# Kernel tuning notes

Hardware: AMD Instinct MI355X
Metric: run time of the kernel (lower is better)

Reference implementation:

```python
import jax, jax.numpy as jnp
import numpy as np

B, N, E, L = 64, 50000, 1600000, 20
BN_EPS = 1e-5


def setup_inputs() -> dict:
    key = jax.random.key(0)
    ks = jax.random.split(key, 8)
    x = jax.random.normal(ks[0], (B, N), dtype=jnp.float32)
    edge_index = jax.random.randint(ks[1], (2, E), 0, N, dtype=jnp.int32)
    alpha = jax.random.normal(ks[2], (E,), dtype=jnp.float32)
    bias = jax.random.normal(ks[3], (E,), dtype=jnp.float32)
    # LazyLinear(num_labels) on [B, N] features
    W = jax.random.normal(ks[4], (L, N), dtype=jnp.float32) / np.sqrt(N)
    b_lin = jax.random.normal(ks[5], (L,), dtype=jnp.float32) * 0.01
    # LazyBatchNorm1d affine params over N features
    gamma = jnp.ones((N,), dtype=jnp.float32)
    beta = jnp.zeros((N,), dtype=jnp.float32)
    return {"x": x, "edge_index": edge_index, "alpha": alpha, "bias": bias,
            "W": W, "b_lin": b_lin, "gamma": gamma, "beta": beta}


def reference(x, edge_index, alpha, bias, W, b_lin, gamma, beta):
    src, dst = edge_index[0], edge_index[1]
    # gather per-edge source features and apply per-edge affine: [B, E]
    x_e = alpha * x[:, src] + bias
    # scatter-mean into destination nodes: [B, N]
    sums = jnp.zeros((x.shape[0], N), dtype=x.dtype).at[:, dst].add(x_e)
    counts = jnp.zeros((N,), dtype=x.dtype).at[dst].add(1.0)
    x_hat = sums / jnp.maximum(counts, 1.0)
    out = jnp.tanh(x_hat)
    # linear head: [B, L]
    pred = x_hat @ W.T + b_lin
    # BatchNorm1d (training mode: batch stats, biased variance)
    mu = jnp.mean(out, axis=0)
    var = jnp.var(out, axis=0)
    bn = (out - mu) / jnp.sqrt(var + BN_EPS) * gamma + beta
    return (pred, bn)
```

## Files before the change

kernel.cpp:

```cpp
#include <hip/hip_runtime.h>
#include <math.h>

#define NB 64
#define NL 20
#define BN_EPS 1e-5f

#define BIN_W 32
#define NBIN 1563
#define NBINP 2048
#define BIN_CAP 1280
#define CHUNK 4096

__device__ __forceinline__ unsigned short f2bf(float f) {
    unsigned u = __float_as_uint(f);
    unsigned r = u + 0x7fff + ((u >> 16) & 1);
    return (unsigned short)(r >> 16);
}
__device__ __forceinline__ float bf2f(unsigned short h) {
    return __uint_as_float(((unsigned)h) << 16);
}

__global__ __launch_bounds__(256) void transpose_kernel(
    const float* __restrict__ x, unsigned short* __restrict__ xTb, int Nn) {
    __shared__ float tile[64][65];
    int n0 = blockIdx.x * 64;
    int ln = threadIdx.x & 63;
    int wv = threadIdx.x >> 6;
    for (int r = wv; r < 64; r += 4) {
        int col = n0 + ln;
        tile[r][ln] = (col < Nn) ? x[r * Nn + col] : 0.f;
    }
    __syncthreads();
    for (int r = wv; r < 64; r += 4) {
        int node = n0 + r;
        if (node < Nn) xTb[(size_t)node * 64 + ln] = f2bf(tile[ln][r]);
    }
}

__global__ __launch_bounds__(1024) void binsort_kernel(
    const int* __restrict__ src, const int* __restrict__ dst,
    const float* __restrict__ alpha, const float* __restrict__ bias,
    int* __restrict__ cursor, uint2* __restrict__ paybins, int E) {
    __shared__ unsigned hist[NBINP];
    __shared__ unsigned gbase[NBINP];

    int tid = threadIdx.x;
    int e0 = blockIdx.x * CHUNK;

    hist[tid] = 0;
    hist[tid + 1024] = 0;
    __syncthreads();

    uint2 pay[4];
    unsigned rk[4];
    int bn[4];
    #pragma unroll
    for (int k = 0; k < 4; ++k) {
        int e = e0 + k * 1024 + tid;
        bn[k] = -1;
        if (e < E) {
            int d = dst[e];
            int b = d >> 5;
            int dl = d & 31;
            pay[k].x = (unsigned)src[e] | ((unsigned)f2bf(alpha[e]) << 16);
            pay[k].y = (unsigned)f2bf(bias[e]) | ((unsigned)dl << 16) |
                       ((unsigned)b << 21);
            bn[k] = b;
            rk[k] = atomicAdd(&hist[b], 1u);
        }
    }
    __syncthreads();

    for (int i = tid; i < NBINP; i += 1024) {
        unsigned v = hist[i];
        if (v > 0) gbase[i] = (unsigned)atomicAdd(&cursor[i], (int)v);
    }
    __syncthreads();

    #pragma unroll
    for (int k = 0; k < 4; ++k) {
        if (bn[k] >= 0) {
            unsigned di = gbase[bn[k]] + rk[k];
            if (di < BIN_CAP)
                paybins[(size_t)bn[k] * BIN_CAP + di] = pay[k];
        }
    }
}

__global__ __launch_bounds__(256) void pull_fin3_kernel(
    const int* __restrict__ cursor, const uint2* __restrict__ paybins,
    const unsigned short* __restrict__ xTb, const float* __restrict__ W,
    const float* __restrict__ gamma, const float* __restrict__ beta,
    float* __restrict__ pred_part, float* __restrict__ bn, int Nn) {
    __shared__ __align__(16) char smem[16640];
    uint2* ed = (uint2*)smem;
    float (*xh)[65] = (float (*)[65])smem;
    float (*th)[65] = (float (*)[65])(smem + 8320);

    __shared__ float wl[NL][32];
    __shared__ unsigned h2[32], b2[32], c2[32];
    __shared__ float mu_s[32], a_s[32], be_s[32];

    int bin = blockIdx.x;
    int tid = threadIdx.x;
    int ln = tid & 63;
    int w = tid >> 6;
    int n0 = bin * 32;

    int cnt = cursor[bin];
    if (cnt > BIN_CAP) cnt = BIN_CAP;
    const uint2* pb = paybins + (size_t)bin * BIN_CAP;

    for (int i = tid; i < NL * 32; i += 256) {
        int l = i >> 5, j = i & 31;
        wl[l][j] = (n0 + j < Nn) ? W[l * Nn + n0 + j] : 0.f;
    }
    if (tid < 32) { h2[tid] = 0; c2[tid] = 0; }
    __syncthreads();

    uint2 pA = {0, 0}, pB = {0, 0}, pC = {0, 0}, pD = {0, 0}, pE = {0, 0};
    {
        int i;
        i = tid;
        if (i < cnt) { pA = pb[i]; atomicAdd(&h2[(pA.y >> 16) & 31], 1u); }
        i = tid + 256;
        if (i < cnt) { pB = pb[i]; atomicAdd(&h2[(pB.y >> 16) & 31], 1u); }
        i = tid + 512;
        if (i < cnt) { pC = pb[i]; atomicAdd(&h2[(pC.y >> 16) & 31], 1u); }
        i = tid + 768;
        if (i < cnt) { pD = pb[i]; atomicAdd(&h2[(pD.y >> 16) & 31], 1u); }
        i = tid + 1024;
        if (i < cnt) { pE = pb[i]; atomicAdd(&h2[(pE.y >> 16) & 31], 1u); }
    }
    __syncthreads();

    if (tid < 32) {
        unsigned v = h2[tid];
        unsigned incl = v;
        #pragma unroll
        for (int off = 1; off < 32; off <<= 1) {
            unsigned t = __shfl_up(incl, off, 64);
            if (tid >= off) incl += t;
        }
        b2[tid] = incl - v;
    }
    __syncthreads();

    {
        if (tid < cnt) {
            unsigned dl = (pA.y >> 16) & 31;
            ed[b2[dl] + atomicAdd(&c2[dl], 1u)] = pA;
        }
        if (tid + 256 < cnt) {
            unsigned dl = (pB.y >> 16) & 31;
            ed[b2[dl] + atomicAdd(&c2[dl], 1u)] = pB;
        }
        if (tid + 512 < cnt) {
            unsigned dl = (pC.y >> 16) & 31;
            ed[b2[dl] + atomicAdd(&c2[dl], 1u)] = pC;
        }
        if (tid + 768 < cnt) {
            unsigned dl = (pD.y >> 16) & 31;
            ed[b2[dl] + atomicAdd(&c2[dl], 1u)] = pD;
        }
        if (tid + 1024 < cnt) {
            unsigned dl = (pE.y >> 16) & 31;
            ed[b2[dl] + atomicAdd(&c2[dl], 1u)] = pE;
        }
    }
    __syncthreads();

    float xh_reg[8], th_reg[8];
    #pragma unroll
    for (int k = 0; k < 8; ++k) {
        int dl = w * 8 + k;
        int node = n0 + dl;
        int n = (int)h2[dl];
        unsigned bs = b2[dl];
        float a0 = 0.f, a1 = 0.f, a2 = 0.f, a3 = 0.f, bsum = 0.f;
        int j = 0;
        for (; j + 3 < n; j += 4) {
            uint2 e0 = ed[bs + j];
            uint2 e1 = ed[bs + j + 1];
            uint2 e2 = ed[bs + j + 2];
            uint2 e3 = ed[bs + j + 3];
            bsum += __uint_as_float((e0.y & 0xffffu) << 16) +
                    __uint_as_float((e1.y & 0xffffu) << 16) +
                    __uint_as_float((e2.y & 0xffffu) << 16) +
                    __uint_as_float((e3.y & 0xffffu) << 16);
            a0 = fmaf(__uint_as_float(e0.x & 0xffff0000u),
                      bf2f(xTb[(size_t)(e0.x & 0xffffu) * 64 + ln]), a0);
            a1 = fmaf(__uint_as_float(e1.x & 0xffff0000u),
                      bf2f(xTb[(size_t)(e1.x & 0xffffu) * 64 + ln]), a1);
            a2 = fmaf(__uint_as_float(e2.x & 0xffff0000u),
                      bf2f(xTb[(size_t)(e2.x & 0xffffu) * 64 + ln]), a2);
            a3 = fmaf(__uint_as_float(e3.x & 0xffff0000u),
                      bf2f(xTb[(size_t)(e3.x & 0xffffu) * 64 + ln]), a3);
        }
        for (; j < n; ++j) {
            uint2 e0 = ed[bs + j];
            bsum += __uint_as_float((e0.y & 0xffffu) << 16);
            a0 = fmaf(__uint_as_float(e0.x & 0xffff0000u),
                      bf2f(xTb[(size_t)(e0.x & 0xffffu) * 64 + ln]), a0);
        }
        float xhat = 0.f;
        if (node < Nn)
            xhat = ((a0 + a1) + (a2 + a3) + bsum) / fmaxf((float)n, 1.0f);
        xh_reg[k] = xhat;
        float tv = tanhf(xhat);
        th_reg[k] = tv;

        float s = tv, q = tv * tv;
        #pragma unroll
        for (int off = 32; off > 0; off >>= 1) {
            s += __shfl_xor(s, off, 64);
            q += __shfl_xor(q, off, 64);
        }
        if (ln == 0) {
            float mu = s * (1.0f / 64.0f);
            float var = fmaxf(q * (1.0f / 64.0f) - mu * mu, 0.f);
            float inv = rsqrtf(var + BN_EPS);
            float gm = 1.f, bt = 0.f;
            if (node < Nn) { gm = gamma[node]; bt = beta[node]; }
            mu_s[dl] = mu;
            a_s[dl] = inv * gm;
            be_s[dl] = bt;
        }
    }
    __syncthreads();

    #pragma unroll
    for (int k = 0; k < 8; ++k) {
        xh[w * 8 + k][ln] = xh_reg[k];
        th[w * 8 + k][ln] = th_reg[k];
    }
    __syncthreads();

    {
        float acc[5] = {0.f, 0.f, 0.f, 0.f, 0.f};
        for (int n = 0; n < 32; ++n) {
            float xv = xh[n][ln];
            #pragma unroll
            for (int k = 0; k < 5; ++k)
                acc[k] = fmaf(xv, wl[w + k * 4][n], acc[k]);
        }
        #pragma unroll
        for (int k = 0; k < 5; ++k)
            pred_part[(size_t)bin * (NB * NL) + ln * NL + (w + k * 4)] = acc[k];
    }

    for (int idx = tid; idx < 32 * 64; idx += 256) {
        int noff = idx & 31, bb = idx >> 5;
        int node = n0 + noff;
        if (node < Nn)
            bn[bb * Nn + node] =
                fmaf(th[noff][bb] - mu_s[noff], a_s[noff], be_s[noff]);
    }
}

__global__ __launch_bounds__(256) void reduce_pred_kernel(
    const float* __restrict__ part, const float* __restrict__ b_lin,
    float* __restrict__ pred, int nblk) {
    int out = blockIdx.x * 4 + (threadIdx.x >> 6);
    if (out >= NB * NL) return;
    int ln = threadIdx.x & 63;
    float s = 0.f;
    for (int i = ln; i < nblk; i += 64)
        s += part[(size_t)i * (NB * NL) + out];
    #pragma unroll
    for (int off = 32; off > 0; off >>= 1)
        s += __shfl_xor(s, off, 64);
    if (ln == 0) pred[out] = b_lin[out % NL] + s;
}

extern "C" void kernel_launch(void* const* d_in, const int* in_sizes, int n_in,
                              void* d_out, int out_size, void* d_ws, size_t ws_size,
                              hipStream_t stream) {
    const float* x     = (const float*)d_in[0];
    const int*   ei    = (const int*)d_in[1];
    const float* alpha = (const float*)d_in[2];
    const float* bias  = (const float*)d_in[3];
    const float* W     = (const float*)d_in[4];
    const float* b_lin = (const float*)d_in[5];
    const float* gamma = (const float*)d_in[6];
    const float* beta  = (const float*)d_in[7];

    const int Nn = in_sizes[0] / NB;
    const int E  = in_sizes[1] / 2;
    const int* src = ei;
    const int* dst = ei + E;

    const int ntile = (Nn + 63) / 64;

    uint2*          paybins = (uint2*)d_ws;
    unsigned short* xTb     = (unsigned short*)(paybins + (size_t)NBIN * BIN_CAP);
    int*            cursor  = (int*)(xTb + (size_t)Nn * 64);
    float*          pred_part = (float*)(cursor + NBIN);

    float* pred = (float*)d_out;
    float* bn   = pred + NB * NL;

    hipMemsetAsync(cursor, 0, NBIN * sizeof(int), stream);

    transpose_kernel<<<ntile, 256, 0, stream>>>(x, xTb, Nn);
    binsort_kernel<<<(E + CHUNK - 1) / CHUNK, 1024, 0, stream>>>(
        src, dst, alpha, bias, cursor, paybins, E);
    pull_fin3_kernel<<<NBIN, 256, 0, stream>>>(cursor, paybins, xTb, W,
                                               gamma, beta, pred_part, bn, Nn);
    reduce_pred_kernel<<<(NB * NL + 3) / 4, 256, 0, stream>>>(
        pred_part, b_lin, pred, NBIN);
}
```

Measured before the change: 194.3 us.

## Split edge binning into two-pass radix scatter via superbins

Replaces the single-pass scatter of edges into 1563 destination bins with two passes. The first pass scatters into 49 coarse superbins of 1024 nodes. The second pass reads each superbin in slices and scatters into the 32 fine bins it contains. The aim is fewer scattered global writes and fewer global atomics per block in exchange for a larger shared-memory-friendly locality. It adds an extra kernel launch, an extra full read/write of the edge payload buffer, and a fixed superbin capacity that could drop edges if exceeded.

```diff
diff --git a/kernel.cpp b/kernel.cpp
--- a/kernel.cpp
+++ b/kernel.cpp
@@ -7,9 +7,13 @@
 
 #define BIN_W 32
 #define NBIN 1563
-#define NBINP 2048
 #define BIN_CAP 1280
 #define CHUNK 4096
+
+#define NSB 49
+#define NSBP 64
+#define CAP1 36864
+#define NSLICE 9
 
 __device__ __forceinline__ unsigned short f2bf(float f) {
     unsigned u = __float_as_uint(f);
@@ -37,27 +41,26 @@
     }
 }
 
-__global__ __launch_bounds__(1024) void binsort_kernel(
+__global__ __launch_bounds__(1024) void binA_kernel(
     const int* __restrict__ src, const int* __restrict__ dst,
     const float* __restrict__ alpha, const float* __restrict__ bias,
-    int* __restrict__ cursor, uint2* __restrict__ paybins, int E) {
-    __shared__ unsigned hist[NBINP];
-    __shared__ unsigned gbase[NBINP];
+    int* __restrict__ cnt1, uint2* __restrict__ buf1, int E) {
+    __shared__ unsigned hist[NSBP];
+    __shared__ unsigned gbase[NSBP];
 
     int tid = threadIdx.x;
     int e0 = blockIdx.x * CHUNK;
 
-    hist[tid] = 0;
-    hist[tid + 1024] = 0;
+    if (tid < NSBP) hist[tid] = 0;
     __syncthreads();
 
     uint2 pay[4];
     unsigned rk[4];
-    int bn[4];
+    int sb[4];
     #pragma unroll
     for (int k = 0; k < 4; ++k) {
         int e = e0 + k * 1024 + tid;
-        bn[k] = -1;
+        sb[k] = -1;
         if (e < E) {
             int d = dst[e];
             int b = d >> 5;
@@ -65,24 +68,77 @@
             pay[k].x = (unsigned)src[e] | ((unsigned)f2bf(alpha[e]) << 16);
             pay[k].y = (unsigned)f2bf(bias[e]) | ((unsigned)dl << 16) |
                        ((unsigned)b << 21);
-            bn[k] = b;
-            rk[k] = atomicAdd(&hist[b], 1u);
-        }
-    }
-    __syncthreads();
-
-    for (int i = tid; i < NBINP; i += 1024) {
-        unsigned v = hist[i];
-        if (v > 0) gbase[i] = (unsigned)atomicAdd(&cursor[i], (int)v);
+            sb[k] = d >> 10;
+            rk[k] = atomicAdd(&hist[sb[k]], 1u);
+        }
+    }
+    __syncthreads();
+
+    if (tid < NSBP) {
+        unsigned v = hist[tid];
+        if (v > 0) gbase[tid] = (unsigned)atomicAdd(&cnt1[tid], (int)v);
     }
     __syncthreads();
 
     #pragma unroll
     for (int k = 0; k < 4; ++k) {
-        if (bn[k] >= 0) {
-            unsigned di = gbase[bn[k]] + rk[k];
+        if (sb[k] >= 0) {
+            unsigned di = gbase[sb[k]] + rk[k];
+            if (di < CAP1)
+                buf1[(size_t)sb[k] * CAP1 + di] = pay[k];
+        }
+    }
+}
+
+__global__ __launch_bounds__(1024) void binB_kernel(
+    const int* __restrict__ cnt1, const uint2* __restrict__ buf1,
+    int* __restrict__ cursor, uint2* __restrict__ paybins) {
+    __shared__ unsigned hist[32];
+    __shared__ unsigned gbase[32];
+
+    int tid = threadIdx.x;
+    int sb = blockIdx.x / NSLICE;
+    int slice = blockIdx.x % NSLICE;
+
+    int lim = cnt1[sb];
+    if (lim > CAP1) lim = CAP1;
+    int cc = lim - slice * 4096;
+    if (cc < 0) cc = 0;
+    if (cc > 4096) cc = 4096;
+    const uint2* pb = buf1 + (size_t)sb * CAP1 + (size_t)slice * 4096;
+
+    if (tid < 32) hist[tid] = 0;
+    __syncthreads();
+
+    uint2 pay[4];
+    unsigned rk[4];
+    int lb[4];
+    #pragma unroll
+    for (int k = 0; k < 4; ++k) {
+        int i = k * 1024 + tid;
+        lb[k] = -1;
+        if (i < cc) {
+            pay[k] = pb[i];
+            lb[k] = (int)((pay[k].y >> 21) & 31u);
+            rk[k] = atomicAdd(&hist[lb[k]], 1u);
+        }
+    }
+    __syncthreads();
+
+    if (tid < 32) {
+        unsigned v = hist[tid];
+        if (v > 0)
+            gbase[tid] = (unsigned)atomicAdd(&cursor[sb * 32 + tid], (int)v);
+    }
+    __syncthreads();
+
+    #pragma unroll
+    for (int k = 0; k < 4; ++k) {
+        if (lb[k] >= 0) {
+            int bin = sb * 32 + lb[k];
+            unsigned di = gbase[lb[k]] + rk[k];
             if (di < BIN_CAP)
-                paybins[(size_t)bn[k] * BIN_CAP + di] = pay[k];
+                paybins[(size_t)bin * BIN_CAP + di] = pay[k];
         }
     }
 }
@@ -293,18 +349,21 @@
     const int ntile = (Nn + 63) / 64;
 
     uint2*          paybins = (uint2*)d_ws;
-    unsigned short* xTb     = (unsigned short*)(paybins + (size_t)NBIN * BIN_CAP);
-    int*            cursor  = (int*)(xTb + (size_t)Nn * 64);
-    float*          pred_part = (float*)(cursor + NBIN);
+    uint2*          buf1    = paybins + (size_t)NBIN * BIN_CAP;
+    float*          pred_part = (float*)buf1;
+    unsigned short* xTb     = (unsigned short*)(buf1 + (size_t)NSB * CAP1);
+    int*            cnt1    = (int*)(xTb + (size_t)Nn * 64);
+    int*            cursor  = cnt1 + NSBP;
 
     float* pred = (float*)d_out;
     float* bn   = pred + NB * NL;
 
-    hipMemsetAsync(cursor, 0, NBIN * sizeof(int), stream);
+    hipMemsetAsync(cnt1, 0, (NSBP + NBIN + 32) * sizeof(int), stream);
 
     transpose_kernel<<<ntile, 256, 0, stream>>>(x, xTb, Nn);
-    binsort_kernel<<<(E + CHUNK - 1) / CHUNK, 1024, 0, stream>>>(
-        src, dst, alpha, bias, cursor, paybins, E);
+    binA_kernel<<<(E + CHUNK - 1) / CHUNK, 1024, 0, stream>>>(
+        src, dst, alpha, bias, cnt1, buf1, E);
+    binB_kernel<<<NSB * NSLICE, 1024, 0, stream>>>(cnt1, buf1, cursor, paybins);
     pull_fin3_kernel<<<NBIN, 256, 0, stream>>>(cursor, paybins, xTb, W,
                                                gamma, beta, pred_part, bn, Nn);
     reduce_pred_kernel<<<(NB * NL + 3) / 4, 256, 0, stream>>>(
```

New measurement: 197.8 us. No clear change (+1.8%).
